# Optimization experiments

Measured on AMD Instinct MI355X. Metric: run time of the kernel, lower is better.

Reference implementation:

```python
import jax, jax.numpy as jnp
import numpy as np
import math

HEADS = 8
GS = 128          # attention group (window) size; key window = 2*GS
NUM_CLASSES = 4
SCALES = (4, 2, 1)  # lf -> mf -> hf (low to high reconstruction)
R_BASE, R_MIN, R_MAX = 0.5, 0.25, 0.75
LAMBDA_P, LAMBDA_V = 0.25, 0.25
NEG = -1e9


def segment_pool_features(x, scores, scale):
    # score-weighted pooling of `scale` consecutive tokens (pad_n==0 since N % scale == 0)
    if scale == 1:
        return x, scores
    b, n, c = x.shape
    xg = x.reshape(b, n // scale, scale, c)
    sg = scores.reshape(b, n // scale, scale)
    w = jnp.clip(sg, 1e-6, None)[..., None]
    pooled = (xg * w).sum(2) / w.sum(2)
    return pooled, sg.mean(2)


def segment_pool_labels(labels, scores, scale):
    # majority vote; ties broken by score mass, then earliest position
    if scale == 1:
        return labels
    b, n = labels.shape
    gl = labels.reshape(b, n // scale, scale)
    gsc = scores.reshape(b, n // scale, scale)
    oh = jax.nn.one_hot(gl, NUM_CLASSES, dtype=scores.dtype)      # (b,g,s,C)
    counts = oh.sum(2)
    ssum = (oh * gsc[..., None]).sum(2)
    cmask = counts == counts.max(-1, keepdims=True)
    ssum = jnp.where(cmask, ssum, NEG)
    smask = ssum == ssum.max(-1, keepdims=True)
    pos = jnp.arange(scale).reshape(1, 1, scale, 1)
    firstp = jnp.where(oh > 0, pos, scale).min(2)                 # (b,g,C)
    firstp = jnp.where(smask, firstp, scale)
    return jnp.argmin(firstp, -1).astype(labels.dtype)


def align_attn_state(prev, target_ng):
    # gs/ws/heads match across levels, so trilinear interp (align_corners=False)
    # reduces to linear interpolation along the group axis, then clamp+renorm.
    b, n, h, q, k = prev.shape
    pos = (jnp.arange(target_ng) + 0.5) * (n / target_ng) - 0.5
    lo = jnp.clip(jnp.floor(pos).astype(jnp.int32), 0, n - 1)
    hi = jnp.clip(lo + 1, 0, n - 1)
    w = jnp.clip(pos - jnp.floor(pos), 0.0, 1.0).astype(prev.dtype)
    w = w.reshape(1, target_ng, 1, 1, 1)
    a = prev[:, lo] * (1 - w) + prev[:, hi] * w
    a = jnp.clip(a, 0.0, None)
    return a / (a.sum(-1, keepdims=True) + 1e-9)


def pfsa(x, labels, scores, prior, Wq, Wk, Wv, Wp, beta_logit):
    # progressive focused sparse attention on overlapping windows
    b, n, dim = x.shape
    q, k, v = x @ Wq, x @ Wk, x @ Wv
    ng = n // GS
    tail = lambda t: jnp.concatenate([t, jnp.flip(t[:, -GS:], axis=1)], axis=1)
    widx = jnp.arange(ng)[:, None] * GS + jnp.arange(2 * GS)[None, :]
    kw = tail(k)[:, widx]                                          # (b,ng,2gs,qk)
    vw = tail(v)[:, widx]
    dqk, dv = Wq.shape[1] // HEADS, dim // HEADS
    qw = q.reshape(b, ng, GS, HEADS, dqk).transpose(0, 1, 3, 2, 4)
    kw = kw.reshape(b, ng, 2 * GS, HEADS, dqk).transpose(0, 1, 3, 2, 4)
    vw = vw.reshape(b, ng, 2 * GS, HEADS, dv).transpose(0, 1, 3, 2, 4)
    sim = jnp.einsum('bghqd,bghkd->bghqk', qw, kw) / math.sqrt(dqk)
    # dynamic focus ratio from label purity and score variance
    qlab = labels.reshape(b, ng, GS)
    qsc = scores.reshape(b, ng, GS)
    oh = jax.nn.one_hot(qlab, NUM_CLASSES, dtype=scores.dtype)
    mode = jnp.argmax(oh.sum(2), -1)                               # (b,ng)
    purity = (qlab == mode[..., None]).astype(scores.dtype).mean(-1)
    svar = jnp.var(qsc, axis=-1)
    focus = jnp.clip(R_BASE + LAMBDA_P * purity - LAMBDA_V * svar, R_MIN, R_MAX)
    keep = jnp.ceil(focus * (2 * GS)).astype(jnp.int32)            # (b,ng)
    ranks = jnp.argsort(jnp.argsort(-sim, axis=-1), axis=-1)
    mask = ranks < keep[:, :, None, None, None]
    attn = jax.nn.softmax(jnp.where(mask, sim, NEG), axis=-1)
    beta = jax.nn.sigmoid(beta_logit)
    if prior is not None:
        attn = (1 - beta) * attn + beta * prior
    out = jnp.einsum('bghqk,bghkd->bghqd', attn, vw)
    out = out.transpose(0, 1, 3, 2, 4).reshape(b, n, dim)
    return out @ Wp, attn


def setup_inputs() -> dict:
    key = jax.random.key(0)
    ks = jax.random.split(key, 10)
    B, N, DIM, QK = 2, 8192, 512, 512
    x = jax.random.normal(ks[0], (B, N, DIM), dtype=jnp.float32)
    labels = jax.random.randint(ks[1], (B, N), 0, NUM_CLASSES, dtype=jnp.int32)
    scores = jax.random.uniform(ks[2], (B, N), dtype=jnp.float32)
    idx_last = jnp.stack([jax.random.permutation(k, N) for k in jax.random.split(ks[3], B)]).astype(jnp.int32)
    s = 0.02
    Wq = jax.random.normal(ks[4], (3, DIM, QK), dtype=jnp.float32) * s
    Wk = jax.random.normal(ks[5], (3, DIM, QK), dtype=jnp.float32) * s
    Wv = jax.random.normal(ks[6], (3, DIM, DIM), dtype=jnp.float32) * s
    Wp = jax.random.normal(ks[7], (3, DIM, DIM), dtype=jnp.float32) * s
    beta_logit = jax.random.normal(ks[8], (3,), dtype=jnp.float32)
    return {"x": x, "labels": labels, "scores": scores, "idx_last": idx_last,
            "Wq": Wq, "Wk": Wk, "Wv": Wv, "Wp": Wp, "beta_logit": beta_logit}


def reference(x, labels, scores, idx_last, Wq, Wk, Wv, Wp, beta_logit):
    b, n, _ = x.shape
    acc = jnp.zeros_like(x)
    prev = None
    for i, scale in enumerate(SCALES):  # low-freq -> high-freq reconstruction
        xl, sl = segment_pool_features(x, scores, scale)
        ll = segment_pool_labels(labels, scores, scale)
        prior = align_attn_state(prev, (n // scale) // GS) if prev is not None else None
        out_l, prev = pfsa(xl, ll, sl, prior, Wq[i], Wk[i], Wv[i], Wp[i], beta_logit[i])
        acc = acc + jnp.repeat(out_l, scale, axis=1)[:, :n]  # repeat_each
    # restore_sorted_tokens: scatter along token dim with per-batch permutation
    restored = jnp.zeros_like(acc).at[jnp.arange(b)[:, None], idx_last].set(acc)
    return restored
```

## Files before the change

kernel.cpp:

```cpp
#include <hip/hip_runtime.h>
#include <math.h>


#define GS   128
#define WIN  256
#define DQK  64
#define DV   64
#define DIMC 512
#define NTOK 8192
#define WSZ  262144

typedef unsigned long long u64;
typedef unsigned short u16;
typedef __attribute__((ext_vector_type(8))) short bf16x8;
typedef __attribute__((ext_vector_type(4))) float f32x4;

__device__ __forceinline__ u16 f2b(float f) {
  unsigned u = __float_as_uint(f);
  u = (u + 0x7fffu + ((u >> 16) & 1u)) >> 16;
  return (u16)u;
}
__device__ __forceinline__ float b2f(u16 h) { return __uint_as_float(((unsigned)h) << 16); }
__device__ __forceinline__ float b2f_lo(unsigned u) { return __uint_as_float(u << 16); }
__device__ __forceinline__ float b2f_hi(unsigned u) { return __uint_as_float(u & 0xffff0000u); }

__device__ __forceinline__ float wave_max64(float v) {
#pragma unroll
  for (int m = 1; m < 64; m <<= 1) v = fmaxf(v, __shfl_xor(v, m, 64));
  return v;
}
__device__ __forceinline__ float wave_sum64(float v) {
#pragma unroll
  for (int m = 1; m < 64; m <<= 1) v += __shfl_xor(v, m, 64);
  return v;
}

__global__ void pool_split01_kernel(const float* __restrict__ x,
                                    const float* __restrict__ scores,
                                    u16* __restrict__ xhi, u16* __restrict__ xlo,
                                    float* __restrict__ sl) {
  int tid = blockIdx.x * 256 + threadIdx.x;
  int scale, npool, rowoff, rest;
  if (tid < 524288) { scale = 4; npool = 2048; rowoff = 0;    rest = tid >> 7; }
  else { tid -= 524288; scale = 2; npool = 4096; rowoff = 4096; rest = tid >> 7; }
  int c4 = tid & 127;
  int g  = rest % npool;
  int b  = rest / npool;
  const float* xp = x + ((size_t)b * NTOK + (size_t)g * scale) * DIMC + c4 * 4;
  float ax = 0.f, ay = 0.f, az = 0.f, aw = 0.f, wsum = 0.f, ssum = 0.f;
  for (int s = 0; s < scale; ++s) {
    float sc = scores[(size_t)b * NTOK + (size_t)g * scale + s];
    float w  = fmaxf(sc, 1e-6f);
    float4 xv = *reinterpret_cast<const float4*>(xp + (size_t)s * DIMC);
    ax += xv.x * w; ay += xv.y * w; az += xv.z * w; aw += xv.w * w;
    wsum += w; ssum += sc;
  }
  float o[4] = { ax / wsum, ay / wsum, az / wsum, aw / wsum };
  ushort4 h, l;
  h.x = f2b(o[0]); h.y = f2b(o[1]); h.z = f2b(o[2]); h.w = f2b(o[3]);
  l.x = f2b(o[0] - b2f(h.x)); l.y = f2b(o[1] - b2f(h.y));
  l.z = f2b(o[2] - b2f(h.z)); l.w = f2b(o[3] - b2f(h.w));
  size_t row = (size_t)rowoff + (size_t)b * npool + g;
  size_t off = row * DIMC + c4 * 4;
  *reinterpret_cast<ushort4*>(xhi + off) = h;
  *reinterpret_cast<ushort4*>(xlo + off) = l;
  if (c4 == 0) sl[row] = ssum / (float)scale;
}

__global__ void pool_label01_kernel(const int* __restrict__ labels,
                                    const float* __restrict__ scores,
                                    int* __restrict__ ll) {
  int tid = blockIdx.x * 256 + threadIdx.x;
  int scale, npool, rowoff;
  if (tid < 4096) { scale = 4; npool = 2048; rowoff = 0; }
  else { tid -= 4096; scale = 2; npool = 4096; rowoff = 4096; }
  int b = tid / npool, g = tid % npool;
  float counts[4] = {0.f, 0.f, 0.f, 0.f};
  float ssum[4]   = {0.f, 0.f, 0.f, 0.f};
  int firstp[4];
  for (int c = 0; c < 4; ++c) firstp[c] = scale;
  for (int s = 0; s < scale; ++s) {
    int   L = labels[(size_t)b * NTOK + (size_t)g * scale + s];
    float S = scores[(size_t)b * NTOK + (size_t)g * scale + s];
    counts[L] += 1.0f;
    ssum[L]   += S;
    if (s < firstp[L]) firstp[L] = s;
  }
  float cmax = fmaxf(fmaxf(counts[0], counts[1]), fmaxf(counts[2], counts[3]));
  float s2[4];
  for (int c = 0; c < 4; ++c) s2[c] = (counts[c] == cmax) ? ssum[c] : -1e9f;
  float smax = fmaxf(fmaxf(s2[0], s2[1]), fmaxf(s2[2], s2[3]));
  int fp[4];
  for (int c = 0; c < 4; ++c) fp[c] = (s2[c] == smax) ? firstp[c] : scale;
  int best = 0, bv = fp[0];
  for (int c = 1; c < 4; ++c) if (fp[c] < bv) { bv = fp[c]; best = c; }
  ll[rowoff + b * npool + g] = best;
}

__global__ void asplit_kernel(const float* __restrict__ x,
                              u16* __restrict__ xhi, u16* __restrict__ xlo) {
  int tid = blockIdx.x * 256 + threadIdx.x;
  float4 v = *reinterpret_cast<const float4*>(x + (size_t)tid * 4);
  ushort4 h, l;
  h.x = f2b(v.x); h.y = f2b(v.y); h.z = f2b(v.z); h.w = f2b(v.w);
  l.x = f2b(v.x - b2f(h.x)); l.y = f2b(v.y - b2f(h.y));
  l.z = f2b(v.z - b2f(h.z)); l.w = f2b(v.w - b2f(h.w));
  *reinterpret_cast<ushort4*>(xhi + (size_t)tid * 4) = h;
  *reinterpret_cast<ushort4*>(xlo + (size_t)tid * 4) = l;
}

__global__ void keep_all_kernel(const int* __restrict__ ll, const float* __restrict__ sl,
                                const int* __restrict__ labels,
                                const float* __restrict__ scores,
                                int* __restrict__ keep) {
  int tid = blockIdx.x * 128 + threadIdx.x;
  if (tid >= 224) return;
  const int* lp; const float* sp;
  if (tid < 32) {
    int b = tid >> 4, g = tid & 15;
    lp = ll + (b * 2048 + g * GS);
    sp = sl + (b * 2048 + g * GS);
  } else if (tid < 96) {
    int e = tid - 32;
    int b = e >> 5, g = e & 31;
    lp = ll + 4096 + (b * 4096 + g * GS);
    sp = sl + 4096 + (b * 4096 + g * GS);
  } else {
    int e = tid - 96;
    int b = e >> 6, g = e & 63;
    lp = labels + ((size_t)b * NTOK + g * GS);
    sp = scores + ((size_t)b * NTOK + g * GS);
  }
  float counts[4] = {0.f, 0.f, 0.f, 0.f};
  for (int i = 0; i < GS; ++i) counts[lp[i]] += 1.f;
  int mode = 0; float bv = counts[0];
  for (int c = 1; c < 4; ++c) if (counts[c] > bv) { bv = counts[c]; mode = c; }
  float pm = 0.f, mean = 0.f;
  for (int i = 0; i < GS; ++i) { pm += (lp[i] == mode) ? 1.f : 0.f; mean += sp[i]; }
  float purity = pm / (float)GS;
  mean /= (float)GS;
  float var = 0.f;
  for (int i = 0; i < GS; ++i) { float d = sp[i] - mean; var += d * d; }
  var /= (float)GS;
  float focus = 0.5f + 0.25f * purity - 0.25f * var;
  focus = fminf(fmaxf(focus, 0.25f), 0.75f);
  keep[tid] = (int)ceilf(focus * (float)WIN);
}

__global__ __launch_bounds__(256) void wprep_kernel(
    const float* __restrict__ Wq, const float* __restrict__ Wk,
    const float* __restrict__ Wv, const float* __restrict__ Wp,
    u16* __restrict__ whiAll, u16* __restrict__ wloAll) {
  __shared__ float tile[32][33];
  int blk = blockIdx.x;
  int mat = blk >> 8;
  int sub = blk & 255;
  int kind = mat / 3, lvl = mat % 3;
  const float* W = (kind == 0 ? Wq : kind == 1 ? Wk : kind == 2 ? Wv : Wp)
                   + (size_t)lvl * WSZ;
  u16* bthi = whiAll + (size_t)mat * WSZ;
  u16* btlo = (mat < 6) ? (wloAll + (size_t)mat * WSZ) : nullptr;

  int bx = sub & 15;
  int by = sub >> 4;
  int tx = threadIdx.x & 31;
  int ty = threadIdx.x >> 5;
#pragma unroll
  for (int i = 0; i < 4; ++i) {
    int kk = ty + i * 8;
    tile[kk][tx] = W[(size_t)(by * 32 + kk) * 512 + bx * 32 + tx];
  }
  __syncthreads();
#pragma unroll
  for (int i = 0; i < 4; ++i) {
    int nn = ty + i * 8;
    float v = tile[tx][nn];
    u16 h = f2b(v);
    size_t o = (size_t)(bx * 32 + nn) * 512 + by * 32 + tx;
    bthi[o] = h;
    if (btlo) btlo[o] = f2b(v - b2f(h));
  }
}

__global__ __launch_bounds__(256) void qkv_gemm_kernel(
    const u16* __restrict__ Ahi, const u16* __restrict__ Alo,
    const u16* __restrict__ whiAll, const u16* __restrict__ wloAll,
    u16* __restrict__ qhi, u16* __restrict__ qlo,
    u16* __restrict__ khi, u16* __restrict__ klo, u16* __restrict__ vbf,
    int lvlA, int lvlB, int ysplit, int rowB) {
  __shared__ u16 smem[4 * 4096];
  u16* sAhi = smem;
  u16* sBhi = smem + 4096;
  u16* sAlo = smem + 2 * 4096;
  u16* sBlo = smem + 3 * 4096;

  int lin = blockIdx.y * 12 + blockIdx.x;
  int n = gridDim.y * 12;
  int swz = (lin & 7) * (n >> 3) + (lin >> 3);
  int xx = swz % 12;
  int ry = swz / 12;
  int sel = xx >> 2;
  int cx  = xx & 3;
  bool split = (sel < 2);
  int lvl   = (ry < ysplit) ? lvlA : lvlB;
  int row0  = (ry < ysplit) ? ry * 128 : rowB + (ry - ysplit) * 128;
  const u16* Bh = whiAll + (size_t)(sel * 3 + lvl) * WSZ;
  const u16* Bl = wloAll + (size_t)(sel * 3 + lvl) * WSZ;

  int t = threadIdx.x, lane = t & 63, wave = t >> 6;
  int wr = wave >> 1, wc = wave & 1;
  int col0 = cx * 128;

  int srow = (lane >> 2);
  int schk = (lane & 3) * 8;

  const f32x4 zero = { 0.f, 0.f, 0.f, 0.f };
  f32x4 acc[4][4];
#pragma unroll
  for (int i = 0; i < 4; ++i)
#pragma unroll
    for (int j = 0; j < 4; ++j) acc[i][j] = zero;

  for (int k0 = 0; k0 < 512; k0 += 32) {
#pragma unroll
    for (int j = 0; j < 2; ++j) {
      int r = wave * 32 + j * 16 + srow;
      const u16* gA = Ahi + (size_t)(row0 + r) * 512 + k0 + schk;
      const u16* gB = Bh + (size_t)(col0 + r) * 512 + k0 + schk;
      __builtin_amdgcn_global_load_lds(
          (const __attribute__((address_space(1))) void*)gA,
          (__attribute__((address_space(3))) void*)&sAhi[(wave * 32 + j * 16) * 32],
          16, 0, 0);
      __builtin_amdgcn_global_load_lds(
          (const __attribute__((address_space(1))) void*)gB,
          (__attribute__((address_space(3))) void*)&sBhi[(wave * 32 + j * 16) * 32],
          16, 0, 0);
      if (split) {
        const u16* gAl = Alo + (size_t)(row0 + r) * 512 + k0 + schk;
        const u16* gBl = Bl + (size_t)(col0 + r) * 512 + k0 + schk;
        __builtin_amdgcn_global_load_lds(
            (const __attribute__((address_space(1))) void*)gAl,
            (__attribute__((address_space(3))) void*)&sAlo[(wave * 32 + j * 16) * 32],
            16, 0, 0);
        __builtin_amdgcn_global_load_lds(
            (const __attribute__((address_space(1))) void*)gBl,
            (__attribute__((address_space(3))) void*)&sBlo[(wave * 32 + j * 16) * 32],
            16, 0, 0);
      }
    }
    __syncthreads();

    int fr = lane & 15;
    int kf = (lane >> 4) * 8;
    bf16x8 ah[4], bh[4], al[4], bl[4];
#pragma unroll
    for (int i = 0; i < 4; ++i) {
      ah[i] = *reinterpret_cast<const bf16x8*>(&sAhi[(wr * 64 + i * 16 + fr) * 32 + kf]);
      bh[i] = *reinterpret_cast<const bf16x8*>(&sBhi[(wc * 64 + i * 16 + fr) * 32 + kf]);
      if (split) {
        al[i] = *reinterpret_cast<const bf16x8*>(&sAlo[(wr * 64 + i * 16 + fr) * 32 + kf]);
        bl[i] = *reinterpret_cast<const bf16x8*>(&sBlo[(wc * 64 + i * 16 + fr) * 32 + kf]);
      }
    }
#pragma unroll
    for (int i = 0; i < 4; ++i)
#pragma unroll
      for (int j = 0; j < 4; ++j) {
        acc[i][j] = __builtin_amdgcn_mfma_f32_16x16x32_bf16(ah[i], bh[j], acc[i][j], 0, 0, 0);
        if (split) {
          acc[i][j] = __builtin_amdgcn_mfma_f32_16x16x32_bf16(ah[i], bl[j], acc[i][j], 0, 0, 0);
          acc[i][j] = __builtin_amdgcn_mfma_f32_16x16x32_bf16(al[i], bh[j], acc[i][j], 0, 0, 0);
        }
      }
    __syncthreads();
  }

  int ccol = col0 + wc * 64 + (lane & 15);
  int crow = row0 + wr * 64 + (lane >> 4) * 4;
  if (sel == 2) {
#pragma unroll
    for (int i = 0; i < 4; ++i)
#pragma unroll
      for (int r = 0; r < 4; ++r) {
        int gr = crow + i * 16 + r;
#pragma unroll
        for (int j = 0; j < 4; ++j)
          vbf[(size_t)gr * 512 + ccol + j * 16] = f2b(acc[i][j][r]);
      }
  } else {
    u16* Ch = (sel == 0) ? qhi : khi;
    u16* Cl = (sel == 0) ? qlo : klo;
#pragma unroll
    for (int i = 0; i < 4; ++i)
#pragma unroll
      for (int r = 0; r < 4; ++r) {
        int gr = crow + i * 16 + r;
#pragma unroll
        for (int j = 0; j < 4; ++j) {
          float v = acc[i][j][r];
          u16 hh = f2b(v);
          Ch[(size_t)gr * 512 + ccol + j * 16] = hh;
          Cl[(size_t)gr * 512 + ccol + j * 16] = f2b(v - b2f(hh));
        }
      }
  }
}

template<int EMODE>
__global__ __launch_bounds__(256) void wp_gemm_kernel(
    const u16* __restrict__ Ahi, const u16* __restrict__ Bthi,
    float* __restrict__ C, const int* __restrict__ idx,
    int M, int scale, int n_l) {
  __shared__ u16 smem[2 * 4096];
  u16* sAhi = smem;
  u16* sBhi = smem + 4096;

  int lin = blockIdx.y * 4 + blockIdx.x;
  int n = gridDim.y * 4;
  int swz = (lin & 7) * (n >> 3) + (lin >> 3);
  int row0 = (swz >> 2) * 128, col0 = (swz & 3) * 128;

  int t = threadIdx.x, lane = t & 63, wave = t >> 6;
  int wr = wave >> 1, wc = wave & 1;

  int srow = (lane >> 2);
  int schk = (lane & 3) * 8;

  const f32x4 zero = { 0.f, 0.f, 0.f, 0.f };
  f32x4 acc[4][4];
#pragma unroll
  for (int i = 0; i < 4; ++i)
#pragma unroll
    for (int j = 0; j < 4; ++j) acc[i][j] = zero;

  for (int k0 = 0; k0 < 512; k0 += 32) {
#pragma unroll
    for (int j = 0; j < 2; ++j) {
      int r = wave * 32 + j * 16 + srow;
      const u16* gA = Ahi + (size_t)(row0 + r) * 512 + k0 + schk;
      const u16* gB = Bthi + (size_t)(col0 + r) * 512 + k0 + schk;
      __builtin_amdgcn_global_load_lds(
          (const __attribute__((address_space(1))) void*)gA,
          (__attribute__((address_space(3))) void*)&sAhi[(wave * 32 + j * 16) * 32],
          16, 0, 0);
      __builtin_amdgcn_global_load_lds(
          (const __attribute__((address_space(1))) void*)gB,
          (__attribute__((address_space(3))) void*)&sBhi[(wave * 32 + j * 16) * 32],
          16, 0, 0);
    }
    __syncthreads();

    int fr = lane & 15;
    int kf = (lane >> 4) * 8;
    bf16x8 ah[4], bh[4];
#pragma unroll
    for (int i = 0; i < 4; ++i) {
      ah[i] = *reinterpret_cast<const bf16x8*>(&sAhi[(wr * 64 + i * 16 + fr) * 32 + kf]);
      bh[i] = *reinterpret_cast<const bf16x8*>(&sBhi[(wc * 64 + i * 16 + fr) * 32 + kf]);
    }
#pragma unroll
    for (int i = 0; i < 4; ++i)
#pragma unroll
      for (int j = 0; j < 4; ++j)
        acc[i][j] = __builtin_amdgcn_mfma_f32_16x16x32_bf16(ah[i], bh[j], acc[i][j], 0, 0, 0);
    __syncthreads();
  }

  int ccol = col0 + wc * 64 + (lane & 15);
  int crow = row0 + wr * 64 + (lane >> 4) * 4;
#pragma unroll
  for (int i = 0; i < 4; ++i) {
#pragma unroll
    for (int r = 0; r < 4; ++r) {
      int gr = crow + i * 16 + r;
      int bb = gr / n_l, rr = gr - bb * n_l;
      for (int s = 0; s < scale; ++s) {
        int dst = idx[(size_t)bb * NTOK + (size_t)rr * scale + s];
        float* p = C + ((size_t)bb * NTOK + dst) * 512 + ccol;
        if (EMODE == 3) {
#pragma unroll
          for (int j = 0; j < 4; ++j) p[j * 16] += acc[i][j][r];
        } else {
#pragma unroll
          for (int j = 0; j < 4; ++j) p[j * 16] = acc[i][j][r];
        }
      }
    }
  }
}

__global__ __launch_bounds__(512) void attn_fused_kernel(
    const u16* __restrict__ qhi, const u16* __restrict__ qlo,
    const u16* __restrict__ khi, const u16* __restrict__ klo,
    const u16* __restrict__ vbf, const int* __restrict__ keepArr,
    const u16* __restrict__ prevA, u16* __restrict__ curA,
    const float* __restrict__ betaL, u16* __restrict__ outp,
    int lvl, int n_l, int ng, int prev_ng) {
  __shared__ u64 smem8[5120];
  u16*   Khi_s  = (u16*)smem8;
  u16*   Klo_s  = Khi_s + 256 * 32;
  u16*   Qhi_s  = Klo_s + 256 * 32;
  u16*   Qlo_s  = Qhi_s + 64 * 32;
  float* S_lds  = (float*)smem8;
  u16*   P_half = (u16*)smem8;
  u16*   Vt     = P_half + 64 * 136;

  int t = threadIdx.x;
  int lane = t & 63, wave = t >> 6;
  int nwg = gridDim.x;
  int bid = (blockIdx.x & 7) * (nwg >> 3) + (blockIdx.x >> 3);
  int p   = bid & 1;
  int h   = (bid >> 1) & 7;
  int gl  = bid >> 4;
  int g   = gl % ng;
  int b   = gl / ng;
  int bgh = bid >> 1;

  const u16* qhbase = qhi + ((size_t)b * n_l + (size_t)g * GS + p * 64) * DIMC + h * DQK;
  const u16* qlbase = qlo + ((size_t)b * n_l + (size_t)g * GS + p * 64) * DIMC + h * DQK;
  const u16* khbase = khi + (size_t)b * n_l * DIMC + h * DQK;
  const u16* klbase = klo + (size_t)b * n_l * DIMC + h * DQK;

  int qt  = wave >> 1;
  int ktb = (wave & 1) * 8;
  f32x4 acc[8];
#pragma unroll
  for (int i = 0; i < 8; ++i) acc[i] = (f32x4){0.f, 0.f, 0.f, 0.f};

#pragma unroll
  for (int dp = 0; dp < 2; ++dp) {
    if (dp) __syncthreads();
    int d0 = dp * 32;
#pragma unroll
    for (int ii = 0; ii < 2; ++ii) {
      int row = wave * 32 + ii * 16 + (lane >> 2);
      int pp = g * GS + row;
      int src = (pp < n_l) ? pp : (2 * n_l - 1 - pp);
      const u16* gH = khbase + (size_t)src * DIMC + d0 + (lane & 3) * 8;
      const u16* gL = klbase + (size_t)src * DIMC + d0 + (lane & 3) * 8;
      __builtin_amdgcn_global_load_lds(
          (const __attribute__((address_space(1))) void*)gH,
          (__attribute__((address_space(3))) void*)&Khi_s[(wave * 32 + ii * 16) * 32],
          16, 0, 0);
      __builtin_amdgcn_global_load_lds(
          (const __attribute__((address_space(1))) void*)gL,
          (__attribute__((address_space(3))) void*)&Klo_s[(wave * 32 + ii * 16) * 32],
          16, 0, 0);
    }
    if (wave < 4) {
      int row = wave * 16 + (lane >> 2);
      const u16* gH = qhbase + (size_t)row * DIMC + d0 + (lane & 3) * 8;
      __builtin_amdgcn_global_load_lds(
          (const __attribute__((address_space(1))) void*)gH,
          (__attribute__((address_space(3))) void*)&Qhi_s[(wave * 16) * 32],
          16, 0, 0);
    } else {
      int row = (wave - 4) * 16 + (lane >> 2);
      const u16* gL = qlbase + (size_t)row * DIMC + d0 + (lane & 3) * 8;
      __builtin_amdgcn_global_load_lds(
          (const __attribute__((address_space(1))) void*)gL,
          (__attribute__((address_space(3))) void*)&Qlo_s[((wave - 4) * 16) * 32],
          16, 0, 0);
    }
    __syncthreads();

    int fr = lane & 15;
    int kf = (lane >> 4) * 8;
    bf16x8 bqh = *reinterpret_cast<const bf16x8*>(&Qhi_s[(qt * 16 + fr) * 32 + kf]);
    bf16x8 bql = *reinterpret_cast<const bf16x8*>(&Qlo_s[(qt * 16 + fr) * 32 + kf]);
    __builtin_amdgcn_s_setprio(1);
#pragma unroll
    for (int kt = 0; kt < 8; ++kt) {
      bf16x8 akh = *reinterpret_cast<const bf16x8*>(&Khi_s[((ktb + kt) * 16 + fr) * 32 + kf]);
      bf16x8 akl = *reinterpret_cast<const bf16x8*>(&Klo_s[((ktb + kt) * 16 + fr) * 32 + kf]);
      acc[kt] = __builtin_amdgcn_mfma_f32_16x16x32_bf16(akh, bqh, acc[kt], 0, 0, 0);
      acc[kt] = __builtin_amdgcn_mfma_f32_16x16x32_bf16(akh, bql, acc[kt], 0, 0, 0);
      acc[kt] = __builtin_amdgcn_mfma_f32_16x16x32_bf16(akl, bqh, acc[kt], 0, 0, 0);
    }
    __builtin_amdgcn_s_setprio(0);
  }
  __syncthreads();

  int kp = keepArr[b * ng + g];
  float beta = 0.f, wgt = 0.f;
  int plo_ = 0, phi_ = 0;
  if (lvl > 0) {
    beta = 1.f / (1.f + expf(-betaL[lvl]));
    float pos = ((float)g + 0.5f) * ((float)prev_ng / (float)ng) - 0.5f;
    float fl = floorf(pos);
    plo_ = (int)fl;
    if (plo_ < 0) plo_ = 0;
    if (plo_ > prev_ng - 1) plo_ = prev_ng - 1;
    phi_ = plo_ + 1; if (phi_ > prev_ng - 1) phi_ = prev_ng - 1;
    wgt = fminf(fmaxf(pos - fl, 0.f), 1.f);
  }
  u64 lmask = (1ull << lane) - 1ull;

  unsigned atp[8][2];
#pragma unroll
  for (int half = 0; half < 2; ++half) {
    if ((wave >> 2) == half) {
      int ql = ((wave >> 1) & 1) * 16 + (lane & 15);
#pragma unroll
      for (int kt = 0; kt < 8; ++kt) {
        int key = (ktb + kt) * 16 + (lane >> 4) * 4;
        *reinterpret_cast<f32x4*>(&S_lds[ql * 264 + key]) = acc[kt];
      }
    }
    __syncthreads();
#pragma unroll
    for (int j = 0; j < 4; ++j) {
      int lrow = wave * 4 + j;
      int i = p * 64 + half * 32 + lrow;
      f32x4 s4 = *reinterpret_cast<const f32x4*>(&S_lds[lrow * 264 + lane * 4]);
      float sv[4];
      unsigned um[4];
#pragma unroll
      for (int e = 0; e < 4; ++e) {
        sv[e] = s4[e] * 0.125f;
        unsigned u = __float_as_uint(sv[e]);
        um[e] = (u & 0x80000000u) ? ~u : (u | 0x80000000u);
      }
      float m = wave_max64(fmaxf(fmaxf(sv[0], sv[1]), fmaxf(sv[2], sv[3])));
      unsigned T = 0u;
      for (int bit = 31; bit >= 0; --bit) {
        unsigned T2 = T | (1u << bit);
        int c = __popcll(__ballot(um[0] >= T2)) + __popcll(__ballot(um[1] >= T2))
              + __popcll(__ballot(um[2] >= T2)) + __popcll(__ballot(um[3] >= T2));
        if (c >= kp) { T = T2; if (c == kp) break; }
      }
      int c_gt = __popcll(__ballot(um[0] > T)) + __popcll(__ballot(um[1] > T))
               + __popcll(__ballot(um[2] > T)) + __popcll(__ballot(um[3] > T));
      u64 beq[4];
#pragma unroll
      for (int e = 0; e < 4; ++e) beq[e] = __ballot(um[e] == T);
      int trbase = __popcll(beq[0] & lmask) + __popcll(beq[1] & lmask)
                 + __popcll(beq[2] & lmask) + __popcll(beq[3] & lmask);
      int need = kp - c_gt;
      bool msk[4];
      int own = 0;
#pragma unroll
      for (int e = 0; e < 4; ++e) {
        bool eq = (um[e] == T);
        msk[e] = (um[e] > T) || (eq && (trbase + own) < need);
        own += eq ? 1 : 0;
      }
      float ez[4], zs = 0.f;
#pragma unroll
      for (int e = 0; e < 4; ++e) { ez[e] = msk[e] ? __expf(sv[e] - m) : 0.f; zs += ez[e]; }
      zs = wave_sum64(zs);
      float at[4];
#pragma unroll
      for (int e = 0; e < 4; ++e) at[e] = ez[e] / zs;
      if (lvl > 0) {
        size_t baseLo = ((((size_t)b * prev_ng + plo_) * 8 + h) * GS + i) * WIN + lane * 4;
        size_t baseHi = ((((size_t)b * prev_ng + phi_) * 8 + h) * GS + i) * WIN + lane * 4;
        uint2 rlo = *reinterpret_cast<const uint2*>(prevA + baseLo);
        uint2 rhi = *reinterpret_cast<const uint2*>(prevA + baseHi);
        float pl[4] = { b2f_lo(rlo.x), b2f_hi(rlo.x), b2f_lo(rlo.y), b2f_hi(rlo.y) };
        float ph[4] = { b2f_lo(rhi.x), b2f_hi(rhi.x), b2f_lo(rhi.y), b2f_hi(rhi.y) };
#pragma unroll
        for (int e = 0; e < 4; ++e) {
          float pr = fmaxf((1.f - wgt) * pl[e] + wgt * ph[e], 0.f);
          at[e] = (1.f - beta) * at[e] + beta * pr;
        }
      }
      atp[half * 4 + j][0] = (unsigned)f2b(at[0]) | ((unsigned)f2b(at[1]) << 16);
      atp[half * 4 + j][1] = (unsigned)f2b(at[2]) | ((unsigned)f2b(at[3]) << 16);
      if (curA != nullptr) {
        uint2 o = { atp[half * 4 + j][0], atp[half * 4 + j][1] };
        *reinterpret_cast<uint2*>(curA + ((size_t)bgh * GS + i) * WIN + lane * 4) = o;
      }
    }
    __syncthreads();
  }

  const u16* vbase = vbf + (size_t)b * n_l * DIMC + h * DV;
  int rf   = wave >> 1;
  int cf0  = (wave & 1) * 2;
  int frow = lane & 15;
  int fk   = (lane >> 4) * 8;
  f32x4 oacc0 = { 0.f, 0.f, 0.f, 0.f };
  f32x4 oacc1 = { 0.f, 0.f, 0.f, 0.f };
  int jlo = t & 15, vd4 = (t >> 4) & 15, jh2 = t >> 8;

#pragma unroll
  for (int jp = 0; jp < 2; ++jp) {
#pragma unroll
    for (int it = 0; it < 4; ++it) {
      int j = (jh2 * 4 + it) * 16 + jlo;
      int pp = g * GS + jp * 128 + j;
      int src = (pp < n_l) ? pp : (2 * n_l - 1 - pp);
      ushort4 vv = *reinterpret_cast<const ushort4*>(vbase + (size_t)src * DIMC + vd4 * 4);
      Vt[(vd4 * 4 + 0) * 136 + j] = vv.x;
      Vt[(vd4 * 4 + 1) * 136 + j] = vv.y;
      Vt[(vd4 * 4 + 2) * 136 + j] = vv.z;
      Vt[(vd4 * 4 + 3) * 136 + j] = vv.w;
    }
    if ((lane >> 5) == jp) {
      int kl = (lane & 31) * 4;
#pragma unroll
      for (int j = 0; j < 4; ++j) {
        uint2 oA = { atp[j][0], atp[j][1] };
        uint2 oB = { atp[4 + j][0], atp[4 + j][1] };
        *reinterpret_cast<uint2*>(&P_half[(wave * 4 + j) * 136 + kl]) = oA;
        *reinterpret_cast<uint2*>(&P_half[(32 + wave * 4 + j) * 136 + kl]) = oB;
      }
    }
    __syncthreads();
    __builtin_amdgcn_s_setprio(1);
#pragma unroll
    for (int ks = 0; ks < 4; ++ks) {
      bf16x8 a  = *reinterpret_cast<const bf16x8*>(&P_half[(rf * 16 + frow) * 136 + ks * 32 + fk]);
      bf16x8 b0 = *reinterpret_cast<const bf16x8*>(&Vt[(cf0 * 16 + frow) * 136 + ks * 32 + fk]);
      bf16x8 b1 = *reinterpret_cast<const bf16x8*>(&Vt[((cf0 + 1) * 16 + frow) * 136 + ks * 32 + fk]);
      oacc0 = __builtin_amdgcn_mfma_f32_16x16x32_bf16(a, b0, oacc0, 0, 0, 0);
      oacc1 = __builtin_amdgcn_mfma_f32_16x16x32_bf16(a, b1, oacc1, 0, 0, 0);
    }
    __builtin_amdgcn_s_setprio(0);
    __syncthreads();
  }

  u16* obase = outp + ((size_t)b * n_l + (size_t)g * GS + p * 64 + rf * 16) * DIMC + h * DV;
#pragma unroll
  for (int rr = 0; rr < 4; ++rr) {
    int qrow = (lane >> 4) * 4 + rr;
    obase[(size_t)qrow * DIMC + cf0 * 16 + frow]       = f2b(oacc0[rr]);
    obase[(size_t)qrow * DIMC + (cf0 + 1) * 16 + frow] = f2b(oacc1[rr]);
  }
}

extern "C" void kernel_launch(void* const* d_in, const int* in_sizes, int n_in,
                              void* d_out, int out_size, void* d_ws, size_t ws_size,
                              hipStream_t stream) {
  (void)in_sizes; (void)n_in; (void)out_size; (void)ws_size;
  const float* x        = (const float*)d_in[0];
  const int*   labels   = (const int*)d_in[1];
  const float* scores   = (const float*)d_in[2];
  const int*   idx_last = (const int*)d_in[3];
  const float* Wq       = (const float*)d_in[4];
  const float* Wk       = (const float*)d_in[5];
  const float* Wv       = (const float*)d_in[6];
  const float* Wp       = (const float*)d_in[7];
  const float* betaL    = (const float*)d_in[8];
  float* out = (float*)d_out;

  char* w = (char*)d_ws;
  size_t off = 0;
  auto take = [&](size_t bytes) -> char* {
    char* p = w + off;
    off += (bytes + 255) & ~(size_t)255;
    return p;
  };
  u16*   qhib   = (u16*)  take(16777216);
  u16*   qlob   = (u16*)  take(16777216);
  u16*   khib   = (u16*)  take(16777216);
  u16*   klob   = (u16*)  take(16777216);
  u16*   vbf    = (u16*)  take(16777216);
  u16*   xhi    = (u16*)  take(16777216);
  u16*   xlo    = (u16*)  take(16777216);
  u16*   attnA  = (u16*)  take(16777216);
  u16*   attnB  = (u16*)  take(33554432);
  u16*   whiAll = (u16*)  take(6291456);
  u16*   wloAll = (u16*)  take(3145728);
  float* sl     = (float*)take(65536);
  int*   ll     = (int*)  take(65536);
  int*   keepb  = (int*)  take(1024);

  const size_t ROW1 = 4096;

  wprep_kernel<<<3072, 256, 0, stream>>>(Wq, Wk, Wv, Wp, whiAll, wloAll);
  pool_split01_kernel<<<6144, 256, 0, stream>>>(x, scores, xhi, xlo, sl);
  pool_label01_kernel<<<48, 256, 0, stream>>>(labels, scores, ll);
  keep_all_kernel<<<2, 128, 0, stream>>>(ll, sl, labels, scores, keepb);

  {
    dim3 gq(12, 96);
    qkv_gemm_kernel<<<gq, 256, 0, stream>>>(xhi, xlo, whiAll, wloAll,
                                            qhib, qlob, khib, klob, vbf,
                                            0, 1, 32, (int)ROW1);
  }

  attn_fused_kernel<<<2 * 16 * 8 * 2, 512, 0, stream>>>(
      qhib, qlob, khib, klob, vbf, keepb, nullptr, attnA,
      betaL, xhi, 0, 2048, 16, 8);
  {
    dim3 gp(4, 32);
    wp_gemm_kernel<2><<<gp, 256, 0, stream>>>(xhi, whiAll + (size_t)9 * WSZ,
                                              out, idx_last, 4096, 4, 2048);
  }

  attn_fused_kernel<<<2 * 32 * 8 * 2, 512, 0, stream>>>(
      qhib + ROW1 * DIMC, qlob + ROW1 * DIMC, khib + ROW1 * DIMC, klob + ROW1 * DIMC,
      vbf + ROW1 * DIMC, keepb + 32, attnA, attnB,
      betaL, xhi + ROW1 * DIMC, 1, 4096, 32, 16);
  {
    dim3 gp(4, 64);
    wp_gemm_kernel<3><<<gp, 256, 0, stream>>>(xhi + ROW1 * DIMC, whiAll + (size_t)10 * WSZ,
                                              out, idx_last, 8192, 2, 4096);
  }

  asplit_kernel<<<(2 * NTOK * 128) / 256, 256, 0, stream>>>(x, xhi, xlo);
  {
    dim3 gq(12, 128);
    qkv_gemm_kernel<<<gq, 256, 0, stream>>>(xhi, xlo, whiAll, wloAll,
                                            qhib, qlob, khib, klob, vbf,
                                            2, 2, 1 << 20, 0);
  }
  attn_fused_kernel<<<2 * 64 * 8 * 2, 512, 0, stream>>>(
      qhib, qlob, khib, klob, vbf, keepb + 96, attnB, nullptr,
      betaL, xhi, 2, 8192, 64, 32);
  {
    dim3 gp(4, 128);
    wp_gemm_kernel<3><<<gp, 256, 0, stream>>>(xhi, whiAll + (size_t)11 * WSZ,
                                              out, idx_last, 16384, 1, 8192);
  }
}
```

Measured before the change: 498.9 us.

## Merge three per-level output projections into one fused GEMM with single scatter

Replaces the three separate Wp projection GEMMs, two of which did read-modify-write scatters into the output, with one kernel that computes all three levels per 128-row tile. The low-resolution levels' partial results are staged through shared memory and broadcast to their repeated rows, and each output row is written once. Buffers are reassigned so that the level 0/1 attention outputs stay live until the end. This removes two launches and the repeated global read-add-write traffic on the output, at the cost of more shared memory and extra load and MFMA work per block.

```diff
diff --git a/kernel.cpp b/kernel.cpp
--- a/kernel.cpp
+++ b/kernel.cpp
@@ -306,84 +306,152 @@
   }
 }
 
-template<int EMODE>
-__global__ __launch_bounds__(256) void wp_gemm_kernel(
-    const u16* __restrict__ Ahi, const u16* __restrict__ Bthi,
-    float* __restrict__ C, const int* __restrict__ idx,
-    int M, int scale, int n_l) {
-  __shared__ u16 smem[2 * 4096];
-  u16* sAhi = smem;
-  u16* sBhi = smem + 4096;
+__global__ __launch_bounds__(256) void wp_merged_kernel(
+    const u16* __restrict__ xOut01, const u16* __restrict__ xOut2,
+    const u16* __restrict__ whiAll, float* __restrict__ out,
+    const int* __restrict__ idx) {
+  __shared__ u64 smem8[6144];
+  u16* sA2 = (u16*)smem8;
+  u16* sA1 = sA2 + 4096;
+  u16* sA0 = sA1 + 2048;
+  u16* sB2 = sA0 + 1024;
+  u16* sB1 = sB2 + 4096;
+  u16* sB0 = sB1 + 4096;
+  float* acc1f = (float*)smem8;
+  float* acc0f = (float*)smem8 + 8192;
 
   int lin = blockIdx.y * 4 + blockIdx.x;
-  int n = gridDim.y * 4;
-  int swz = (lin & 7) * (n >> 3) + (lin >> 3);
-  int row0 = (swz >> 2) * 128, col0 = (swz & 3) * 128;
+  int swz = (lin & 7) * 64 + (lin >> 3);
+  int ry = swz >> 2, cx = swz & 3;
+  int col0 = cx * 128;
+  int i0  = ry * 128;
+  int bb  = i0 >> 13;
+  int il0 = i0 & 8191;
+  const u16* A2 = xOut2 + (size_t)i0 * 512;
+  const u16* A1 = xOut01 + (size_t)(4096 + bb * 4096 + (il0 >> 1)) * 512;
+  const u16* A0 = xOut01 + (size_t)(bb * 2048 + (il0 >> 2)) * 512;
+  const u16* B2 = whiAll + (size_t)11 * WSZ;
+  const u16* B1 = whiAll + (size_t)10 * WSZ;
+  const u16* B0 = whiAll + (size_t)9  * WSZ;
 
   int t = threadIdx.x, lane = t & 63, wave = t >> 6;
   int wr = wave >> 1, wc = wave & 1;
-
-  int srow = (lane >> 2);
-  int schk = (lane & 3) * 8;
+  int srow = lane >> 2, schk = (lane & 3) * 8;
 
   const f32x4 zero = { 0.f, 0.f, 0.f, 0.f };
-  f32x4 acc[4][4];
+  f32x4 acc2[4][4], acc1[2][4], acc0[4];
 #pragma unroll
   for (int i = 0; i < 4; ++i)
 #pragma unroll
-    for (int j = 0; j < 4; ++j) acc[i][j] = zero;
+    for (int j = 0; j < 4; ++j) acc2[i][j] = zero;
+#pragma unroll
+  for (int i = 0; i < 2; ++i)
+#pragma unroll
+    for (int j = 0; j < 4; ++j) acc1[i][j] = zero;
+#pragma unroll
+  for (int j = 0; j < 4; ++j) acc0[j] = zero;
 
   for (int k0 = 0; k0 < 512; k0 += 32) {
 #pragma unroll
     for (int j = 0; j < 2; ++j) {
       int r = wave * 32 + j * 16 + srow;
-      const u16* gA = Ahi + (size_t)(row0 + r) * 512 + k0 + schk;
-      const u16* gB = Bthi + (size_t)(col0 + r) * 512 + k0 + schk;
-      __builtin_amdgcn_global_load_lds(
-          (const __attribute__((address_space(1))) void*)gA,
-          (__attribute__((address_space(3))) void*)&sAhi[(wave * 32 + j * 16) * 32],
-          16, 0, 0);
-      __builtin_amdgcn_global_load_lds(
-          (const __attribute__((address_space(1))) void*)gB,
-          (__attribute__((address_space(3))) void*)&sBhi[(wave * 32 + j * 16) * 32],
-          16, 0, 0);
+      __builtin_amdgcn_global_load_lds(
+          (const __attribute__((address_space(1))) void*)(A2 + (size_t)r * 512 + k0 + schk),
+          (__attribute__((address_space(3))) void*)&sA2[(wave * 32 + j * 16) * 32], 16, 0, 0);
+      __builtin_amdgcn_global_load_lds(
+          (const __attribute__((address_space(1))) void*)(B2 + (size_t)(col0 + r) * 512 + k0 + schk),
+          (__attribute__((address_space(3))) void*)&sB2[(wave * 32 + j * 16) * 32], 16, 0, 0);
+      __builtin_amdgcn_global_load_lds(
+          (const __attribute__((address_space(1))) void*)(B1 + (size_t)(col0 + r) * 512 + k0 + schk),
+          (__attribute__((address_space(3))) void*)&sB1[(wave * 32 + j * 16) * 32], 16, 0, 0);
+      __builtin_amdgcn_global_load_lds(
+          (const __attribute__((address_space(1))) void*)(B0 + (size_t)(col0 + r) * 512 + k0 + schk),
+          (__attribute__((address_space(3))) void*)&sB0[(wave * 32 + j * 16) * 32], 16, 0, 0);
+    }
+    {
+      int r = wave * 16 + srow;
+      __builtin_amdgcn_global_load_lds(
+          (const __attribute__((address_space(1))) void*)(A1 + (size_t)r * 512 + k0 + schk),
+          (__attribute__((address_space(3))) void*)&sA1[(wave * 16) * 32], 16, 0, 0);
+    }
+    if (wave < 2) {
+      int r = wave * 16 + srow;
+      __builtin_amdgcn_global_load_lds(
+          (const __attribute__((address_space(1))) void*)(A0 + (size_t)r * 512 + k0 + schk),
+          (__attribute__((address_space(3))) void*)&sA0[(wave * 16) * 32], 16, 0, 0);
     }
     __syncthreads();
 
     int fr = lane & 15;
     int kf = (lane >> 4) * 8;
-    bf16x8 ah[4], bh[4];
-#pragma unroll
-    for (int i = 0; i < 4; ++i) {
-      ah[i] = *reinterpret_cast<const bf16x8*>(&sAhi[(wr * 64 + i * 16 + fr) * 32 + kf]);
-      bh[i] = *reinterpret_cast<const bf16x8*>(&sBhi[(wc * 64 + i * 16 + fr) * 32 + kf]);
-    }
-#pragma unroll
-    for (int i = 0; i < 4; ++i)
+    {
+      bf16x8 a[4], b[4];
+#pragma unroll
+      for (int i = 0; i < 4; ++i) {
+        a[i] = *reinterpret_cast<const bf16x8*>(&sA2[(wr * 64 + i * 16 + fr) * 32 + kf]);
+        b[i] = *reinterpret_cast<const bf16x8*>(&sB2[(wc * 64 + i * 16 + fr) * 32 + kf]);
+      }
+#pragma unroll
+      for (int i = 0; i < 4; ++i)
+#pragma unroll
+        for (int j = 0; j < 4; ++j)
+          acc2[i][j] = __builtin_amdgcn_mfma_f32_16x16x32_bf16(a[i], b[j], acc2[i][j], 0, 0, 0);
+    }
+    {
+      bf16x8 a[2], b[4];
+#pragma unroll
+      for (int i = 0; i < 2; ++i)
+        a[i] = *reinterpret_cast<const bf16x8*>(&sA1[(wr * 32 + i * 16 + fr) * 32 + kf]);
 #pragma unroll
       for (int j = 0; j < 4; ++j)
-        acc[i][j] = __builtin_amdgcn_mfma_f32_16x16x32_bf16(ah[i], bh[j], acc[i][j], 0, 0, 0);
-    __syncthreads();
-  }
-
-  int ccol = col0 + wc * 64 + (lane & 15);
-  int crow = row0 + wr * 64 + (lane >> 4) * 4;
+        b[j] = *reinterpret_cast<const bf16x8*>(&sB1[(wc * 64 + j * 16 + fr) * 32 + kf]);
+#pragma unroll
+      for (int i = 0; i < 2; ++i)
+#pragma unroll
+        for (int j = 0; j < 4; ++j)
+          acc1[i][j] = __builtin_amdgcn_mfma_f32_16x16x32_bf16(a[i], b[j], acc1[i][j], 0, 0, 0);
+    }
+    {
+      bf16x8 a = *reinterpret_cast<const bf16x8*>(&sA0[(wr * 16 + fr) * 32 + kf]);
+      bf16x8 b[4];
+#pragma unroll
+      for (int j = 0; j < 4; ++j)
+        b[j] = *reinterpret_cast<const bf16x8*>(&sB0[(wc * 64 + j * 16 + fr) * 32 + kf]);
+#pragma unroll
+      for (int j = 0; j < 4; ++j)
+        acc0[j] = __builtin_amdgcn_mfma_f32_16x16x32_bf16(a, b[j], acc0[j], 0, 0, 0);
+    }
+    __syncthreads();
+  }
+
+  int rbase = (lane >> 4) * 4;
+  int lcb = wc * 64 + (lane & 15);
+#pragma unroll
+  for (int i = 0; i < 2; ++i)
+#pragma unroll
+    for (int j = 0; j < 4; ++j)
+#pragma unroll
+      for (int rr = 0; rr < 4; ++rr)
+        acc1f[(wr * 32 + i * 16 + rbase + rr) * 128 + lcb + j * 16] = acc1[i][j][rr];
+#pragma unroll
+  for (int j = 0; j < 4; ++j)
+#pragma unroll
+    for (int rr = 0; rr < 4; ++rr)
+      acc0f[(wr * 16 + rbase + rr) * 128 + lcb + j * 16] = acc0[j][rr];
+  __syncthreads();
+
 #pragma unroll
   for (int i = 0; i < 4; ++i) {
 #pragma unroll
-    for (int r = 0; r < 4; ++r) {
-      int gr = crow + i * 16 + r;
-      int bb = gr / n_l, rr = gr - bb * n_l;
-      for (int s = 0; s < scale; ++s) {
-        int dst = idx[(size_t)bb * NTOK + (size_t)rr * scale + s];
-        float* p = C + ((size_t)bb * NTOK + dst) * 512 + ccol;
-        if (EMODE == 3) {
-#pragma unroll
-          for (int j = 0; j < 4; ++j) p[j * 16] += acc[i][j][r];
-        } else {
-#pragma unroll
-          for (int j = 0; j < 4; ++j) p[j * 16] = acc[i][j][r];
-        }
+    for (int rr = 0; rr < 4; ++rr) {
+      int grl = wr * 64 + i * 16 + rbase + rr;
+      int dst = idx[(size_t)bb * NTOK + (il0 + grl)];
+      float* p = out + ((size_t)bb * NTOK + dst) * 512 + col0;
+#pragma unroll
+      for (int j = 0; j < 4; ++j) {
+        int lcol = lcb + j * 16;
+        p[lcol] = acc2[i][j][rr] + acc1f[(grl >> 1) * 128 + lcol]
+                                 + acc0f[(grl >> 2) * 128 + lcol];
       }
     }
   }
@@ -661,6 +729,7 @@
   u16*   xlo    = (u16*)  take(16777216);
   u16*   attnA  = (u16*)  take(16777216);
   u16*   attnB  = (u16*)  take(33554432);
+  u16*   x2lo   = (u16*)  take(16777216);
   u16*   whiAll = (u16*)  take(6291456);
   u16*   wloAll = (u16*)  take(3145728);
   float* sl     = (float*)take(65536);
@@ -684,35 +753,25 @@
   attn_fused_kernel<<<2 * 16 * 8 * 2, 512, 0, stream>>>(
       qhib, qlob, khib, klob, vbf, keepb, nullptr, attnA,
       betaL, xhi, 0, 2048, 16, 8);
-  {
-    dim3 gp(4, 32);
-    wp_gemm_kernel<2><<<gp, 256, 0, stream>>>(xhi, whiAll + (size_t)9 * WSZ,
-                                              out, idx_last, 4096, 4, 2048);
-  }
 
   attn_fused_kernel<<<2 * 32 * 8 * 2, 512, 0, stream>>>(
       qhib + ROW1 * DIMC, qlob + ROW1 * DIMC, khib + ROW1 * DIMC, klob + ROW1 * DIMC,
       vbf + ROW1 * DIMC, keepb + 32, attnA, attnB,
       betaL, xhi + ROW1 * DIMC, 1, 4096, 32, 16);
-  {
-    dim3 gp(4, 64);
-    wp_gemm_kernel<3><<<gp, 256, 0, stream>>>(xhi + ROW1 * DIMC, whiAll + (size_t)10 * WSZ,
-                                              out, idx_last, 8192, 2, 4096);
-  }
-
-  asplit_kernel<<<(2 * NTOK * 128) / 256, 256, 0, stream>>>(x, xhi, xlo);
+
+  asplit_kernel<<<(2 * NTOK * 128) / 256, 256, 0, stream>>>(x, attnA, x2lo);
   {
     dim3 gq(12, 128);
-    qkv_gemm_kernel<<<gq, 256, 0, stream>>>(xhi, xlo, whiAll, wloAll,
+    qkv_gemm_kernel<<<gq, 256, 0, stream>>>(attnA, x2lo, whiAll, wloAll,
                                             qhib, qlob, khib, klob, vbf,
                                             2, 2, 1 << 20, 0);
   }
   attn_fused_kernel<<<2 * 64 * 8 * 2, 512, 0, stream>>>(
       qhib, qlob, khib, klob, vbf, keepb + 96, attnB, nullptr,
-      betaL, xhi, 2, 8192, 64, 32);
+      betaL, attnA, 2, 8192, 64, 32);
+
   {
     dim3 gp(4, 128);
-    wp_gemm_kernel<3><<<gp, 256, 0, stream>>>(xhi, whiAll + (size_t)11 * WSZ,
-                                              out, idx_last, 16384, 1, 8192);
-  }
-}
+    wp_merged_kernel<<<gp, 256, 0, stream>>>(xhi, attnA, whiAll, out, idx_last);
+  }
+}
```

After: 444.7 us. 1.12x faster.
